# Performance work log

Measured on AMD Instinct MI355X. Metric: run time of the kernel, lower is better.

Reference implementation:

```python
import jax, jax.numpy as jnp
from jax import lax
import numpy as np

B, T, NX, NXS, NY, NYS, H = 4096, 60, 4, 3, 4, 3, 128


def lstm(x, h0, c0, Wih, Whh, bih, bhh):
    """PyTorch-convention LSTM. x: [B,T,D] -> (hs [B,T,H], hT, cT). Gate order i,f,g,o."""
    xg = jnp.einsum('btd,gd->btg', x, Wih) + bih  # [B,T,4H] precomputed input gates

    def step(carry, xg_t):
        h, c = carry
        g = xg_t + h @ Whh.T + bhh
        i, f, gg, o = jnp.split(g, 4, axis=-1)
        c = jax.nn.sigmoid(f) * c + jax.nn.sigmoid(i) * jnp.tanh(gg)
        h = jax.nn.sigmoid(o) * jnp.tanh(c)
        return (h, c), h

    (hT, cT), hs = lax.scan(step, (h0, c0), jnp.swapaxes(xg, 0, 1))
    return jnp.swapaxes(hs, 0, 1), hT, cT


def setup_inputs() -> dict:
    key = jax.random.key(0)
    ks = jax.random.split(key, 24)
    s = 0.1  # weight init scale
    inp = {
        'inputs_main': jax.random.normal(ks[0], (B, T, NX), jnp.float32),
        'inputs_sfc': jax.random.normal(ks[1], (B, NXS), jnp.float32),
        'rnn1_mem': jax.random.normal(ks[2], (B, T, H), jnp.float32),
        'hx2': jax.random.normal(ks[3], (B, H), jnp.float32),
        'cx2': jax.random.normal(ks[4], (B, H), jnp.float32),
        # surface MLPs -> initial h/c of rnn1
        'W_sfc1': s * jax.random.normal(ks[5], (H, NXS), jnp.float32),
        'b_sfc1': s * jax.random.normal(ks[6], (H,), jnp.float32),
        'W_sfc2': s * jax.random.normal(ks[7], (H, NXS), jnp.float32),
        'b_sfc2': s * jax.random.normal(ks[8], (H,), jnp.float32),
        # rnn1: input dim nx + nh_mem = 4 + 128 = 132
        'Wih1': s * jax.random.normal(ks[9], (4 * H, NX + H), jnp.float32),
        'Whh1': s * jax.random.normal(ks[10], (4 * H, H), jnp.float32),
        'bih1': s * jax.random.normal(ks[11], (4 * H,), jnp.float32),
        'bhh1': s * jax.random.normal(ks[12], (4 * H,), jnp.float32),
        # rnn2: input dim H
        'Wih2': s * jax.random.normal(ks[13], (4 * H, H), jnp.float32),
        'Whh2': s * jax.random.normal(ks[14], (4 * H, H), jnp.float32),
        'bih2': s * jax.random.normal(ks[15], (4 * H,), jnp.float32),
        'bhh2': s * jax.random.normal(ks[16], (4 * H,), jnp.float32),
        # intermediate + output MLPs
        'W_lat': s * jax.random.normal(ks[17], (H, H), jnp.float32),
        'b_lat': s * jax.random.normal(ks[18], (H,), jnp.float32),
        'W_out': s * jax.random.normal(ks[19], (NY, H), jnp.float32),
        'b_out': s * jax.random.normal(ks[20], (NY,), jnp.float32),
        'W_so': s * jax.random.normal(ks[21], (NYS, H), jnp.float32),
        'b_so': s * jax.random.normal(ks[22], (NYS,), jnp.float32),
    }
    return inp


def reference(inputs_main, inputs_sfc, rnn1_mem, hx2, cx2,
              W_sfc1, b_sfc1, W_sfc2, b_sfc2,
              Wih1, Whh1, bih1, bhh1,
              Wih2, Whh2, bih2, bhh2,
              W_lat, b_lat, W_out, b_out, W_so, b_so):
    # initial states of rnn1 from surface features
    hx = jnp.tanh(inputs_sfc @ W_sfc1.T + b_sfc1)
    cx = jnp.tanh(inputs_sfc @ W_sfc2.T + b_sfc2)
    # flip vertical levels, concat memory feedback
    x = jnp.flip(inputs_main, axis=1)
    x = jnp.concatenate([x, rnn1_mem], axis=2)  # [B,T,NX+H]
    rnn1out, _, _ = lstm(x, hx, cx, Wih1, Whh1, bih1, bhh1)
    rnn1out = jnp.flip(rnn1out, axis=1)
    # second LSTM over the opposite direction, random initial state
    rnn2out, last_h, _ = lstm(rnn1out, hx2, cx2, Wih2, Whh2, bih2, bhh2)
    # intermediate mlp (also becomes next-step memory in the stateful module)
    lat = rnn2out @ W_lat.T + b_lat  # [B,T,H]
    out = lat @ W_out.T + b_out      # [B,T,NY]
    out_sfc = last_h @ W_so.T + b_so  # [B,NYS]
    return out, out_sfc
```

## Files before the change

### kernel.cpp

```cpp
#include <hip/hip_runtime.h>
#include <stdint.h>


typedef __bf16 bf16x8 __attribute__((ext_vector_type(8)));
typedef __bf16 bf16x4 __attribute__((ext_vector_type(4)));
typedef float  f32x4  __attribute__((ext_vector_type(4)));

#define HQ      4096u
#define H0_OFF  0u
#define XD_OFF  8192u
#define XA_OFF  24576u
#define LDS_SZ  32256

#define S1f (-1.4426950408889634f)
#define S2f (-2.8853900817779268f)

__device__ __forceinline__ bf16x8 ldw8s(const float* __restrict__ p, float s){
  float4 a = *(const float4*)p;
  float4 b = *(const float4*)(p+4);
  bf16x8 r;
  r[0]=(__bf16)(a.x*s); r[1]=(__bf16)(a.y*s); r[2]=(__bf16)(a.z*s); r[3]=(__bf16)(a.w*s);
  r[4]=(__bf16)(b.x*s); r[5]=(__bf16)(b.y*s); r[6]=(__bf16)(b.z*s); r[7]=(__bf16)(b.w*s);
  return r;
}
__device__ __forceinline__ void load_wgate(bf16x8 (&dst)[8], const float* pih, const float* phh, int gg, float s){
  #pragma unroll
  for (int kk=0;kk<4;++kk) dst[kk]   = ldw8s(pih + kk*32 + gg*8, s);
  #pragma unroll
  for (int kk=0;kk<4;++kk) dst[4+kk] = ldw8s(phh + kk*32 + gg*8, s);
}
__device__ __forceinline__ void step_barrier(){
  asm volatile("s_waitcnt lgkmcnt(0)\n\ts_barrier" ::: "memory");
}
__device__ __forceinline__ void lstm_pw(const f32x4& a0, const f32x4& a1,
                                        const f32x4& a2, const f32x4& a3,
                                        float (&c_)[4], float (&hn)[4]){
  #pragma unroll
  for (int i=0;i<4;++i){
    float ei = __builtin_amdgcn_exp2f(a0[i]);
    float ef = __builtin_amdgcn_exp2f(a1[i]);
    float eg = __builtin_amdgcn_exp2f(fminf(a2[i], 126.0f));
    float eo = __builtin_amdgcn_exp2f(a3[i]);
    float sf = __builtin_amdgcn_rcpf(1.0f + ef);
    float itg = (1.0f - eg) * __builtin_amdgcn_rcpf((1.0f + ei)*(1.0f + eg));
    float ci = sf*c_[i] + itg;
    float ec = __builtin_amdgcn_exp2f(S2f*__builtin_fabsf(ci));
    float th = (1.0f - ec) * __builtin_amdgcn_rcpf((1.0f + eo)*(1.0f + ec));
    c_[i] = ci;
    hn[i] = __builtin_copysignf(th, ci);
  }
}

__global__ void comb_kernel(const float* __restrict__ W_lat, const float* __restrict__ b_lat,
                            const float* __restrict__ W_out, const float* __restrict__ b_out,
                            float* __restrict__ wcomb){
  int tid = threadIdx.x;
  int m = tid >> 7, k = tid & 127;
  float s = 0.f;
  for (int a=0;a<128;++a) s += W_out[m*128+a]*W_lat[a*128+k];
  wcomb[tid] = s;
  if (tid < 4){
    float sb = b_out[tid];
    for (int a=0;a<128;++a) sb += W_out[tid*128+a]*b_lat[a];
    wcomb[512+tid] = sb;
  }
}

#define MF(af_,wb_,ac_) ac_ = __builtin_amdgcn_mfma_f32_16x16x32_bf16(af_, wb_, ac_, 0,0,0)
#define BC8(q_) __builtin_bit_cast(bf16x8, q_)

#define BODY2(T_, CUR_, X0_,X1_,X2_,X3_) { \
    const uint32_t Hc_ = H0_OFF + (uint32_t)(CUR_)*HQ; \
    uint4 qh0_ = *(const uint4*)(lds + Hc_ + ((abase       ) ^ amask)); \
    uint4 qh1_ = *(const uint4*)(lds + Hc_ + ((abase +  64u) ^ amask)); \
    uint4 qh2_ = *(const uint4*)(lds + Hc_ + ((abase + 128u) ^ amask)); \
    uint4 qh3_ = *(const uint4*)(lds + Hc_ + ((abase + 192u) ^ amask)); \
    f32x4 a0 = biasv0, a1 = biasv1, a2 = biasv2, a3 = biasv3; \
    MF(BC8(X0_),wB0[0],a0); MF(BC8(X0_),wB1[0],a1); MF(BC8(X0_),wB2[0],a2); MF(BC8(X0_),wB3[0],a3); \
    MF(BC8(X1_),wB0[1],a0); MF(BC8(X1_),wB1[1],a1); MF(BC8(X1_),wB2[1],a2); MF(BC8(X1_),wB3[1],a3); \
    MF(BC8(X2_),wB0[2],a0); MF(BC8(X2_),wB1[2],a1); MF(BC8(X2_),wB2[2],a2); MF(BC8(X2_),wB3[2],a3); \
    MF(BC8(X3_),wB0[3],a0); MF(BC8(X3_),wB1[3],a1); MF(BC8(X3_),wB2[3],a2); MF(BC8(X3_),wB3[3],a3); \
    if ((T_) <= 57){ \
      const char* xp_ = wsb + (size_t)(57-(T_))*4096u + xfoff; \
      X0_ = *(const uint4*)(xp_);      X1_ = *(const uint4*)(xp_+64); \
      X2_ = *(const uint4*)(xp_+128);  X3_ = *(const uint4*)(xp_+192); \
    } \
    bf16x8 h0_ = BC8(qh0_), h1_ = BC8(qh1_), h2_ = BC8(qh2_), h3_ = BC8(qh3_); \
    MF(h0_,wB0[4],a0); MF(h0_,wB1[4],a1); MF(h0_,wB2[4],a2); MF(h0_,wB3[4],a3); \
    MF(h1_,wB0[5],a0); MF(h1_,wB1[5],a1); MF(h1_,wB2[5],a2); MF(h1_,wB3[5],a3); \
    MF(h2_,wB0[6],a0); MF(h2_,wB1[6],a1); MF(h2_,wB2[6],a2); MF(h2_,wB3[6],a3); \
    MF(h3_,wB0[7],a0); MF(h3_,wB1[7],a1); MF(h3_,wB2[7],a2); MF(h3_,wB3[7],a3); \
    f32x4 ao_ = {0.f,0.f,0.f,0.f}; \
    if (w == 0){ MF(h0_,wcB[0],ao_); MF(h1_,wcB[1],ao_); MF(h2_,wcB[2],ao_); MF(h3_,wcB[3],ao_); } \
    float hn_[4]; \
    lstm_pw(a0,a1,a2,a3, c_, hn_); \
    if ((T_) > 0 && w == 0 && l16 < 4){ \
      _Pragma("unroll") \
      for (int i_=0;i_<4;++i_) \
        dout[(size_t)(b0 + gg*4 + i_)*240 + (size_t)((T_)-1)*4 + l16] = ao_[i_] + bc; \
    } \
    _Pragma("unroll") \
    for (int i_=0;i_<4;++i_) \
      *(__bf16*)(lds + H0_OFF + (uint32_t)(1-(CUR_))*HQ + hw_off[i_]) = (__bf16)hn_[i_]; \
    step_barrier(); \
  }

__global__ __launch_bounds__(512, 2)
void lstm_fused(const float* __restrict__ xmain_g, const float* __restrict__ sfc,
                const float* __restrict__ mem_g, const float* __restrict__ hx2g,
                const float* __restrict__ cx2g,
                const float* __restrict__ Wsfc1, const float* __restrict__ bsfc1,
                const float* __restrict__ Wsfc2, const float* __restrict__ bsfc2,
                const float* __restrict__ Wih1, const float* __restrict__ Whh1,
                const float* __restrict__ bih1, const float* __restrict__ bhh1,
                const float* __restrict__ Wih2, const float* __restrict__ Whh2,
                const float* __restrict__ bih2, const float* __restrict__ bhh2,
                const float* __restrict__ Wso, const float* __restrict__ bso,
                const float* __restrict__ wcomb_ws,
                uint2* __restrict__ ws_u2, float* __restrict__ dout)
{
  __shared__ __align__(16) unsigned char lds[LDS_SZ];
  const int tid = threadIdx.x;
  const int w   = tid >> 6;
  const int l   = tid & 63;
  const int gg  = l >> 4;
  const int l16 = l & 15;
  const int blk = blockIdx.x;
  const int b0  = blk * 16;
  const int j   = (w<<4) + l16;
  const uint32_t amask = (uint32_t)((l16 & 7) << 4);
  const uint32_t abase = (uint32_t)(l16*256 + gg*16);
  const int srow = tid >> 5;
  const uint32_t stg_off = (uint32_t)(((srow*256) + (tid&31)*8) ^ ((srow&7)<<4));
  uint32_t hw_off[4];
  #pragma unroll
  for (int i=0;i<4;++i){
    int r = gg*4 + i;
    hw_off[i] = (uint32_t)((r*256 + j*2) ^ ((r&7)<<4));
  }
  uint2* wsimg = ws_u2 + (size_t)blk * 30720;
  const uint32_t imgoff = (uint32_t)(srow*32 + (tid&31));
  const char* wsb = (const char*)(ws_u2 + (size_t)blk * 30720);
  const uint32_t xfoff = (uint32_t)(l16*256 + gg*16);

  #pragma unroll
  for (int e = tid; e < 960; e += 512){
    int t = e >> 4, row = e & 15;
    float4 xv = *(const float4*)(xmain_g + (size_t)(b0+row)*240 + t*4);
    bf16x4 b4; b4[0]=(__bf16)xv.x; b4[1]=(__bf16)xv.y; b4[2]=(__bf16)xv.z; b4[3]=(__bf16)xv.w;
    *(bf16x4*)(lds + XA_OFF + (uint32_t)e*8u) = b4;
  }
  const float* memrow = mem_g + (size_t)(b0 + srow)*7680 + (tid&31)*4;
  {
    float4 m0 = *(const float4*)memrow;
    float4 m1 = *(const float4*)(memrow + 128);
    bf16x4 a4; a4[0]=(__bf16)m0.x; a4[1]=(__bf16)m0.y; a4[2]=(__bf16)m0.z; a4[3]=(__bf16)m0.w;
    bf16x4 b4; b4[0]=(__bf16)m1.x; b4[1]=(__bf16)m1.y; b4[2]=(__bf16)m1.z; b4[3]=(__bf16)m1.w;
    *(bf16x4*)(lds + XD_OFF + stg_off) = a4;
    *(bf16x4*)(lds + XD_OFF + HQ + stg_off) = b4;
  }
  {
    int c0 = (tid&31)*4;
    float4 wa = *(const float4*)(Wsfc1 + c0*3);
    float4 wb = *(const float4*)(Wsfc1 + c0*3 + 4);
    float4 wc = *(const float4*)(Wsfc1 + c0*3 + 8);
    const float* sp = sfc + (size_t)(b0+srow)*3;
    float s0 = sp[0], s1 = sp[1], s2 = sp[2];
    float4 bb = *(const float4*)(bsfc1 + c0);
    float v0 = tanhf(bb.x + s0*wa.x + s1*wa.y + s2*wa.z);
    float v1 = tanhf(bb.y + s0*wa.w + s1*wb.x + s2*wb.y);
    float v2 = tanhf(bb.z + s0*wb.z + s1*wb.w + s2*wc.x);
    float v3 = tanhf(bb.w + s0*wc.y + s1*wc.z + s2*wc.w);
    bf16x4 h4; h4[0]=(__bf16)v0; h4[1]=(__bf16)v1; h4[2]=(__bf16)v2; h4[3]=(__bf16)v3;
    *(bf16x4*)(lds + H0_OFF + stg_off) = h4;
  }
  float c_[4];
  {
    const float* wr = Wsfc2 + j*3;
    float w0_=wr[0], w1_=wr[1], w2_=wr[2];
    float bj = bsfc2[j];
    #pragma unroll
    for (int i=0;i<4;++i){
      const float* sp = sfc + (size_t)(b0 + gg*4 + i)*3;
      c_[i] = tanhf(bj + sp[0]*w0_ + sp[1]*w1_ + sp[2]*w2_);
    }
  }
  bf16x8 wB0[8], wB1[8], wB2[8], wB3[8];
  load_wgate(wB0, Wih1 + 4 + (size_t)(0*128+j)*132, Whh1 + (size_t)(0*128+j)*128, gg, S1f);
  load_wgate(wB1, Wih1 + 4 + (size_t)(1*128+j)*132, Whh1 + (size_t)(1*128+j)*128, gg, S1f);
  load_wgate(wB2, Wih1 + 4 + (size_t)(2*128+j)*132, Whh1 + (size_t)(2*128+j)*128, gg, S2f);
  load_wgate(wB3, Wih1 + 4 + (size_t)(3*128+j)*132, Whh1 + (size_t)(3*128+j)*128, gg, S1f);
  bf16x8 wxB0 = {}, wxB1 = {}, wxB2 = {}, wxB3 = {};
  if (gg == 0){
    float4 x0 = *(const float4*)(Wih1 + (size_t)(0*128+j)*132);
    float4 x1 = *(const float4*)(Wih1 + (size_t)(1*128+j)*132);
    float4 x2 = *(const float4*)(Wih1 + (size_t)(2*128+j)*132);
    float4 x3 = *(const float4*)(Wih1 + (size_t)(3*128+j)*132);
    wxB0[0]=(__bf16)(x0.x*S1f); wxB0[1]=(__bf16)(x0.y*S1f); wxB0[2]=(__bf16)(x0.z*S1f); wxB0[3]=(__bf16)(x0.w*S1f);
    wxB1[0]=(__bf16)(x1.x*S1f); wxB1[1]=(__bf16)(x1.y*S1f); wxB1[2]=(__bf16)(x1.z*S1f); wxB1[3]=(__bf16)(x1.w*S1f);
    wxB2[0]=(__bf16)(x2.x*S2f); wxB2[1]=(__bf16)(x2.y*S2f); wxB2[2]=(__bf16)(x2.z*S2f); wxB2[3]=(__bf16)(x2.w*S2f);
    wxB3[0]=(__bf16)(x3.x*S1f); wxB3[1]=(__bf16)(x3.y*S1f); wxB3[2]=(__bf16)(x3.z*S1f); wxB3[3]=(__bf16)(x3.w*S1f);
  }
  float bias0 = (bih1[0*128+j] + bhh1[0*128+j])*S1f;
  float bias1 = (bih1[1*128+j] + bhh1[1*128+j])*S1f;
  float bias2 = (bih1[2*128+j] + bhh1[2*128+j])*S2f;
  float bias3 = (bih1[3*128+j] + bhh1[3*128+j])*S1f;
  f32x4 biasv0 = {bias0,bias0,bias0,bias0};
  f32x4 biasv1 = {bias1,bias1,bias1,bias1};
  f32x4 biasv2 = {bias2,bias2,bias2,bias2};
  f32x4 biasv3 = {bias3,bias3,bias3,bias3};
  float4 P0 = *(const float4*)(memrow + 2*128);
  float4 P1 = *(const float4*)(memrow + 3*128);
  step_barrier();

  #pragma unroll 1
  for (int t=0; t<60; ++t){
    const uint32_t cur = (uint32_t)(t & 1);
    const uint32_t Hc = H0_OFF + cur*HQ;
    const uint32_t xb = XD_OFF + (uint32_t)(t & 3)*HQ;
    uint4 qx0 = *(const uint4*)(lds + xb + ((abase       ) ^ amask));
    uint4 qx1 = *(const uint4*)(lds + xb + ((abase +  64u) ^ amask));
    uint4 qx2 = *(const uint4*)(lds + xb + ((abase + 128u) ^ amask));
    uint4 qx3 = *(const uint4*)(lds + xb + ((abase + 192u) ^ amask));
    uint4 qh0 = *(const uint4*)(lds + Hc + ((abase       ) ^ amask));
    uint4 qh1 = *(const uint4*)(lds + Hc + ((abase +  64u) ^ amask));
    uint4 qh2 = *(const uint4*)(lds + Hc + ((abase + 128u) ^ amask));
    uint4 qh3 = *(const uint4*)(lds + Hc + ((abase + 192u) ^ amask));
    uint2 hv  = *(const uint2*)(lds + Hc + stg_off);
    bf16x8 xa = {};
    if (gg == 0){
      bf16x4 x4 = *(const bf16x4*)(lds + XA_OFF + (uint32_t)(((59-t)<<4) + l16)*8u);
      xa[0]=x4[0]; xa[1]=x4[1]; xa[2]=x4[2]; xa[3]=x4[3];
    }
    f32x4 a0 = biasv0, a1 = biasv1, a2 = biasv2, a3 = biasv3;
    MF(xa,wxB0,a0); MF(xa,wxB1,a1); MF(xa,wxB2,a2); MF(xa,wxB3,a3);
    MF(BC8(qx0),wB0[0],a0); MF(BC8(qx0),wB1[0],a1); MF(BC8(qx0),wB2[0],a2); MF(BC8(qx0),wB3[0],a3);
    MF(BC8(qx1),wB0[1],a0); MF(BC8(qx1),wB1[1],a1); MF(BC8(qx1),wB2[1],a2); MF(BC8(qx1),wB3[1],a3);
    MF(BC8(qx2),wB0[2],a0); MF(BC8(qx2),wB1[2],a1); MF(BC8(qx2),wB2[2],a2); MF(BC8(qx2),wB3[2],a3);
    MF(BC8(qx3),wB0[3],a0); MF(BC8(qx3),wB1[3],a1); MF(BC8(qx3),wB2[3],a2); MF(BC8(qx3),wB3[3],a3);
    bf16x8 h0 = BC8(qh0), h1 = BC8(qh1), h2 = BC8(qh2), h3 = BC8(qh3);
    MF(h0,wB0[4],a0); MF(h0,wB1[4],a1); MF(h0,wB2[4],a2); MF(h0,wB3[4],a3);
    MF(h1,wB0[5],a0); MF(h1,wB1[5],a1); MF(h1,wB2[5],a2); MF(h1,wB3[5],a3);
    MF(h2,wB0[6],a0); MF(h2,wB1[6],a1); MF(h2,wB2[6],a2); MF(h2,wB3[6],a3);
    MF(h3,wB0[7],a0); MF(h3,wB1[7],a1); MF(h3,wB2[7],a2); MF(h3,wB3[7],a3);
    float hn[4];
    lstm_pw(a0,a1,a2,a3, c_, hn);
    if (t >= 1) wsimg[(size_t)(t-1)*512 + imgoff] = hv;
    if (t + 2 <= 59){
      bf16x4 m4; m4[0]=(__bf16)P0.x; m4[1]=(__bf16)P0.y; m4[2]=(__bf16)P0.z; m4[3]=(__bf16)P0.w;
      *(bf16x4*)(lds + XD_OFF + (uint32_t)((t+2)&3)*HQ + stg_off) = m4;
    }
    #pragma unroll
    for (int i=0;i<4;++i)
      *(__bf16*)(lds + H0_OFF + (1u-cur)*HQ + hw_off[i]) = (__bf16)hn[i];
    P0 = P1;
    if (t + 4 <= 59) P1 = *(const float4*)(memrow + (size_t)(t+4)*128);
    step_barrier();
  }
  {
    uint2 hv = *(const uint2*)(lds + H0_OFF + stg_off);
    wsimg[(size_t)59*512 + imgoff] = hv;
    float4 h2v = *(const float4*)(hx2g + (size_t)(b0+srow)*128 + (tid&31)*4);
    bf16x4 h4; h4[0]=(__bf16)h2v.x; h4[1]=(__bf16)h2v.y; h4[2]=(__bf16)h2v.z; h4[3]=(__bf16)h2v.w;
    *(bf16x4*)(lds + H0_OFF + stg_off) = h4;
  }
  #pragma unroll
  for (int i=0;i<4;++i) c_[i] = cx2g[(size_t)(b0 + gg*4 + i)*128 + j];
  load_wgate(wB0, Wih2 + (size_t)(0*128+j)*128, Whh2 + (size_t)(0*128+j)*128, gg, S1f);
  load_wgate(wB1, Wih2 + (size_t)(1*128+j)*128, Whh2 + (size_t)(1*128+j)*128, gg, S1f);
  load_wgate(wB2, Wih2 + (size_t)(2*128+j)*128, Whh2 + (size_t)(2*128+j)*128, gg, S2f);
  load_wgate(wB3, Wih2 + (size_t)(3*128+j)*128, Whh2 + (size_t)(3*128+j)*128, gg, S1f);
  {
    float nb0 = (bih2[0*128+j] + bhh2[0*128+j])*S1f;
    float nb1 = (bih2[1*128+j] + bhh2[1*128+j])*S1f;
    float nb2 = (bih2[2*128+j] + bhh2[2*128+j])*S2f;
    float nb3 = (bih2[3*128+j] + bhh2[3*128+j])*S1f;
    biasv0 = (f32x4){nb0,nb0,nb0,nb0};
    biasv1 = (f32x4){nb1,nb1,nb1,nb1};
    biasv2 = (f32x4){nb2,nb2,nb2,nb2};
    biasv3 = (f32x4){nb3,nb3,nb3,nb3};
  }
  bf16x8 wcB[4] = {};
  if (w == 0){
    #pragma unroll
    for (int kk=0;kk<4;++kk){
      bf16x8 v = {};
      if (l16 < 4) v = ldw8s(wcomb_ws + l16*128 + kk*32 + gg*8, 1.0f);
      wcB[kk] = v;
    }
  }
  const float bc = (l16 < 4) ? wcomb_ws[512 + l16] : 0.f;
  asm volatile("s_waitcnt vmcnt(0) lgkmcnt(0)" ::: "memory");
  __builtin_amdgcn_s_barrier();

  uint4 xA0, xA1, xA2, xA3, xB0t, xB1t, xB2t, xB3t;
  {
    const char* pa = wsb + (size_t)59*4096u + xfoff;
    const char* pb = wsb + (size_t)58*4096u + xfoff;
    xA0 = *(const uint4*)(pa);     xA1 = *(const uint4*)(pa+64);
    xA2 = *(const uint4*)(pa+128); xA3 = *(const uint4*)(pa+192);
    xB0t = *(const uint4*)(pb);     xB1t = *(const uint4*)(pb+64);
    xB2t = *(const uint4*)(pb+128); xB3t = *(const uint4*)(pb+192);
  }

  #pragma unroll 1
  for (int tb = 0; tb < 60; tb += 2){
    BODY2(tb,   0, xA0,xA1,xA2,xA3)
    BODY2(tb+1, 1, xB0t,xB1t,xB2t,xB3t)
  }

  if (w == 0){
    bf16x8 wsB[4];
    #pragma unroll
    for (int kk=0;kk<4;++kk){
      bf16x8 v = {};
      if (l16 < 3) v = ldw8s(Wso + l16*128 + kk*32 + gg*8, 1.0f);
      wsB[kk] = v;
    }
    f32x4 ao = {0.f,0.f,0.f,0.f};
    f32x4 as_ = {0.f,0.f,0.f,0.f};
    #pragma unroll
    for (int kk=0;kk<4;++kk){
      uint4 q = *(const uint4*)(lds + H0_OFF + ((abase + 64u*(uint32_t)kk) ^ amask));
      bf16x8 af = BC8(q);
      MF(af, wcB[kk], ao);
      MF(af, wsB[kk], as_);
    }
    if (l16 < 4){
      #pragma unroll
      for (int i=0;i<4;++i)
        dout[(size_t)(b0 + gg*4 + i)*240 + 59*4 + l16] = ao[i] + bc;
    }
    if (l16 < 3){
      float bs = bso[l16];
      #pragma unroll
      for (int i=0;i<4;++i)
        dout[983040 + (size_t)(b0 + gg*4 + i)*3 + l16] = as_[i] + bs;
    }
  }
}

extern "C" void kernel_launch(void* const* d_in, const int* in_sizes, int n_in,
                              void* d_out, int out_size, void* d_ws, size_t ws_size,
                              hipStream_t stream){
  const float* inputs_main = (const float*)d_in[0];
  const float* inputs_sfc  = (const float*)d_in[1];
  const float* rnn1_mem    = (const float*)d_in[2];
  const float* hx2  = (const float*)d_in[3];
  const float* cx2  = (const float*)d_in[4];
  const float* W_sfc1 = (const float*)d_in[5];
  const float* b_sfc1 = (const float*)d_in[6];
  const float* W_sfc2 = (const float*)d_in[7];
  const float* b_sfc2 = (const float*)d_in[8];
  const float* Wih1 = (const float*)d_in[9];
  const float* Whh1 = (const float*)d_in[10];
  const float* bih1 = (const float*)d_in[11];
  const float* bhh1 = (const float*)d_in[12];
  const float* Wih2 = (const float*)d_in[13];
  const float* Whh2 = (const float*)d_in[14];
  const float* bih2 = (const float*)d_in[15];
  const float* bhh2 = (const float*)d_in[16];
  const float* W_lat = (const float*)d_in[17];
  const float* b_lat = (const float*)d_in[18];
  const float* W_out = (const float*)d_in[19];
  const float* b_out = (const float*)d_in[20];
  const float* W_so  = (const float*)d_in[21];
  const float* b_so  = (const float*)d_in[22];
  float* out = (float*)d_out;
  uint2* ws_u2 = (uint2*)d_ws;
  float* wcomb = (float*)((char*)d_ws + 62914560u);

  comb_kernel<<<dim3(1), dim3(512), 0, stream>>>(W_lat, b_lat, W_out, b_out, wcomb);
  lstm_fused<<<dim3(256), dim3(512), 0, stream>>>(inputs_main, inputs_sfc, rnn1_mem, hx2, cx2,
      W_sfc1, b_sfc1, W_sfc2, b_sfc2, Wih1, Whh1, bih1, bhh1, Wih2, Whh2, bih2, bhh2,
      W_so, b_so, wcomb, ws_u2, out);
}
```

Before: 228.0 us.

## Split block into recurrent and input-projection warp groups with LDS handoff

Doubles the block to 1024 threads. Warps 0-7 run only the recurrent h·Whh matmul and the pointwise update. Warps 8-15 precompute the next step's input-gate partials (x·Wih + bias) into a double-buffered LDS region, and also handle memory staging, the workspace writes and the output projection. The goal is to take the input-projection MFMAs off the serial critical path of each timestep. In exchange it uses much more LDS (about 104KB), allows only one block per CU instead of two, and adds an f32 partial round trip through LDS every step.

```diff
diff --git a/kernel.cpp b/kernel.cpp
--- a/kernel.cpp
+++ b/kernel.cpp
@@ -8,9 +8,12 @@
 
 #define HQ      4096u
 #define H0_OFF  0u
-#define XD_OFF  8192u
-#define XA_OFF  24576u
-#define LDS_SZ  32256
+#define PART    8192u
+#define PHALF   32768u
+#define XD_OFF  73728u
+#define XA_OFF  90112u
+#define WC_OFF  97792u
+#define LDS_SZ  105984
 
 #define S1f (-1.4426950408889634f)
 #define S2f (-2.8853900817779268f)
@@ -23,11 +26,9 @@
   r[4]=(__bf16)(b.x*s); r[5]=(__bf16)(b.y*s); r[6]=(__bf16)(b.z*s); r[7]=(__bf16)(b.w*s);
   return r;
 }
-__device__ __forceinline__ void load_wgate(bf16x8 (&dst)[8], const float* pih, const float* phh, int gg, float s){
+__device__ __forceinline__ void load_w4(bf16x8 (&dst)[4], const float* __restrict__ p, int gg, float s){
   #pragma unroll
-  for (int kk=0;kk<4;++kk) dst[kk]   = ldw8s(pih + kk*32 + gg*8, s);
-  #pragma unroll
-  for (int kk=0;kk<4;++kk) dst[4+kk] = ldw8s(phh + kk*32 + gg*8, s);
+  for (int kk=0;kk<4;++kk) dst[kk] = ldw8s(p + kk*32 + gg*8, s);
 }
 __device__ __forceinline__ void step_barrier(){
   asm volatile("s_waitcnt lgkmcnt(0)\n\ts_barrier" ::: "memory");
@@ -69,43 +70,7 @@
 #define MF(af_,wb_,ac_) ac_ = __builtin_amdgcn_mfma_f32_16x16x32_bf16(af_, wb_, ac_, 0,0,0)
 #define BC8(q_) __builtin_bit_cast(bf16x8, q_)
 
-#define BODY2(T_, CUR_, X0_,X1_,X2_,X3_) { \
-    const uint32_t Hc_ = H0_OFF + (uint32_t)(CUR_)*HQ; \
-    uint4 qh0_ = *(const uint4*)(lds + Hc_ + ((abase       ) ^ amask)); \
-    uint4 qh1_ = *(const uint4*)(lds + Hc_ + ((abase +  64u) ^ amask)); \
-    uint4 qh2_ = *(const uint4*)(lds + Hc_ + ((abase + 128u) ^ amask)); \
-    uint4 qh3_ = *(const uint4*)(lds + Hc_ + ((abase + 192u) ^ amask)); \
-    f32x4 a0 = biasv0, a1 = biasv1, a2 = biasv2, a3 = biasv3; \
-    MF(BC8(X0_),wB0[0],a0); MF(BC8(X0_),wB1[0],a1); MF(BC8(X0_),wB2[0],a2); MF(BC8(X0_),wB3[0],a3); \
-    MF(BC8(X1_),wB0[1],a0); MF(BC8(X1_),wB1[1],a1); MF(BC8(X1_),wB2[1],a2); MF(BC8(X1_),wB3[1],a3); \
-    MF(BC8(X2_),wB0[2],a0); MF(BC8(X2_),wB1[2],a1); MF(BC8(X2_),wB2[2],a2); MF(BC8(X2_),wB3[2],a3); \
-    MF(BC8(X3_),wB0[3],a0); MF(BC8(X3_),wB1[3],a1); MF(BC8(X3_),wB2[3],a2); MF(BC8(X3_),wB3[3],a3); \
-    if ((T_) <= 57){ \
-      const char* xp_ = wsb + (size_t)(57-(T_))*4096u + xfoff; \
-      X0_ = *(const uint4*)(xp_);      X1_ = *(const uint4*)(xp_+64); \
-      X2_ = *(const uint4*)(xp_+128);  X3_ = *(const uint4*)(xp_+192); \
-    } \
-    bf16x8 h0_ = BC8(qh0_), h1_ = BC8(qh1_), h2_ = BC8(qh2_), h3_ = BC8(qh3_); \
-    MF(h0_,wB0[4],a0); MF(h0_,wB1[4],a1); MF(h0_,wB2[4],a2); MF(h0_,wB3[4],a3); \
-    MF(h1_,wB0[5],a0); MF(h1_,wB1[5],a1); MF(h1_,wB2[5],a2); MF(h1_,wB3[5],a3); \
-    MF(h2_,wB0[6],a0); MF(h2_,wB1[6],a1); MF(h2_,wB2[6],a2); MF(h2_,wB3[6],a3); \
-    MF(h3_,wB0[7],a0); MF(h3_,wB1[7],a1); MF(h3_,wB2[7],a2); MF(h3_,wB3[7],a3); \
-    f32x4 ao_ = {0.f,0.f,0.f,0.f}; \
-    if (w == 0){ MF(h0_,wcB[0],ao_); MF(h1_,wcB[1],ao_); MF(h2_,wcB[2],ao_); MF(h3_,wcB[3],ao_); } \
-    float hn_[4]; \
-    lstm_pw(a0,a1,a2,a3, c_, hn_); \
-    if ((T_) > 0 && w == 0 && l16 < 4){ \
-      _Pragma("unroll") \
-      for (int i_=0;i_<4;++i_) \
-        dout[(size_t)(b0 + gg*4 + i_)*240 + (size_t)((T_)-1)*4 + l16] = ao_[i_] + bc; \
-    } \
-    _Pragma("unroll") \
-    for (int i_=0;i_<4;++i_) \
-      *(__bf16*)(lds + H0_OFF + (uint32_t)(1-(CUR_))*HQ + hw_off[i_]) = (__bf16)hn_[i_]; \
-    step_barrier(); \
-  }
-
-__global__ __launch_bounds__(512, 2)
+__global__ __launch_bounds__(1024, 1)
 void lstm_fused(const float* __restrict__ xmain_g, const float* __restrict__ sfc,
                 const float* __restrict__ mem_g, const float* __restrict__ hx2g,
                 const float* __restrict__ cx2g,
@@ -127,215 +92,322 @@
   const int l16 = l & 15;
   const int blk = blockIdx.x;
   const int b0  = blk * 16;
-  const int j   = (w<<4) + l16;
   const uint32_t amask = (uint32_t)((l16 & 7) << 4);
   const uint32_t abase = (uint32_t)(l16*256 + gg*16);
-  const int srow = tid >> 5;
-  const uint32_t stg_off = (uint32_t)(((srow*256) + (tid&31)*8) ^ ((srow&7)<<4));
-  uint32_t hw_off[4];
+  uint2* wsimg = ws_u2 + (size_t)blk * 30720;
+  const char* wsb = (const char*)wsimg;
+
   #pragma unroll
-  for (int i=0;i<4;++i){
-    int r = gg*4 + i;
-    hw_off[i] = (uint32_t)((r*256 + j*2) ^ ((r&7)<<4));
-  }
-  uint2* wsimg = ws_u2 + (size_t)blk * 30720;
-  const uint32_t imgoff = (uint32_t)(srow*32 + (tid&31));
-  const char* wsb = (const char*)(ws_u2 + (size_t)blk * 30720);
-  const uint32_t xfoff = (uint32_t)(l16*256 + gg*16);
-
-  #pragma unroll
-  for (int e = tid; e < 960; e += 512){
+  for (int e = tid; e < 960; e += 1024){
     int t = e >> 4, row = e & 15;
     float4 xv = *(const float4*)(xmain_g + (size_t)(b0+row)*240 + t*4);
     bf16x4 b4; b4[0]=(__bf16)xv.x; b4[1]=(__bf16)xv.y; b4[2]=(__bf16)xv.z; b4[3]=(__bf16)xv.w;
     *(bf16x4*)(lds + XA_OFF + (uint32_t)e*8u) = b4;
   }
-  const float* memrow = mem_g + (size_t)(b0 + srow)*7680 + (tid&31)*4;
-  {
-    float4 m0 = *(const float4*)memrow;
-    float4 m1 = *(const float4*)(memrow + 128);
-    bf16x4 a4; a4[0]=(__bf16)m0.x; a4[1]=(__bf16)m0.y; a4[2]=(__bf16)m0.z; a4[3]=(__bf16)m0.w;
-    bf16x4 b4; b4[0]=(__bf16)m1.x; b4[1]=(__bf16)m1.y; b4[2]=(__bf16)m1.z; b4[3]=(__bf16)m1.w;
-    *(bf16x4*)(lds + XD_OFF + stg_off) = a4;
-    *(bf16x4*)(lds + XD_OFF + HQ + stg_off) = b4;
-  }
-  {
-    int c0 = (tid&31)*4;
-    float4 wa = *(const float4*)(Wsfc1 + c0*3);
-    float4 wb = *(const float4*)(Wsfc1 + c0*3 + 4);
-    float4 wc = *(const float4*)(Wsfc1 + c0*3 + 8);
-    const float* sp = sfc + (size_t)(b0+srow)*3;
-    float s0 = sp[0], s1 = sp[1], s2 = sp[2];
-    float4 bb = *(const float4*)(bsfc1 + c0);
-    float v0 = tanhf(bb.x + s0*wa.x + s1*wa.y + s2*wa.z);
-    float v1 = tanhf(bb.y + s0*wa.w + s1*wb.x + s2*wb.y);
-    float v2 = tanhf(bb.z + s0*wb.z + s1*wb.w + s2*wc.x);
-    float v3 = tanhf(bb.w + s0*wc.y + s1*wc.z + s2*wc.w);
-    bf16x4 h4; h4[0]=(__bf16)v0; h4[1]=(__bf16)v1; h4[2]=(__bf16)v2; h4[3]=(__bf16)v3;
-    *(bf16x4*)(lds + H0_OFF + stg_off) = h4;
-  }
-  float c_[4];
-  {
-    const float* wr = Wsfc2 + j*3;
-    float w0_=wr[0], w1_=wr[1], w2_=wr[2];
-    float bj = bsfc2[j];
+
+  if (tid < 512){
+    const int j = w*16 + l16;
+    const int srow = tid >> 5;
+    const uint32_t stg_off = (uint32_t)(((srow*256) + (tid&31)*8) ^ ((srow&7)<<4));
+    uint32_t hw_off[4];
     #pragma unroll
     for (int i=0;i<4;++i){
-      const float* sp = sfc + (size_t)(b0 + gg*4 + i)*3;
-      c_[i] = tanhf(bj + sp[0]*w0_ + sp[1]*w1_ + sp[2]*w2_);
-    }
-  }
-  bf16x8 wB0[8], wB1[8], wB2[8], wB3[8];
-  load_wgate(wB0, Wih1 + 4 + (size_t)(0*128+j)*132, Whh1 + (size_t)(0*128+j)*128, gg, S1f);
-  load_wgate(wB1, Wih1 + 4 + (size_t)(1*128+j)*132, Whh1 + (size_t)(1*128+j)*128, gg, S1f);
-  load_wgate(wB2, Wih1 + 4 + (size_t)(2*128+j)*132, Whh1 + (size_t)(2*128+j)*128, gg, S2f);
-  load_wgate(wB3, Wih1 + 4 + (size_t)(3*128+j)*132, Whh1 + (size_t)(3*128+j)*128, gg, S1f);
-  bf16x8 wxB0 = {}, wxB1 = {}, wxB2 = {}, wxB3 = {};
-  if (gg == 0){
-    float4 x0 = *(const float4*)(Wih1 + (size_t)(0*128+j)*132);
-    float4 x1 = *(const float4*)(Wih1 + (size_t)(1*128+j)*132);
-    float4 x2 = *(const float4*)(Wih1 + (size_t)(2*128+j)*132);
-    float4 x3 = *(const float4*)(Wih1 + (size_t)(3*128+j)*132);
-    wxB0[0]=(__bf16)(x0.x*S1f); wxB0[1]=(__bf16)(x0.y*S1f); wxB0[2]=(__bf16)(x0.z*S1f); wxB0[3]=(__bf16)(x0.w*S1f);
-    wxB1[0]=(__bf16)(x1.x*S1f); wxB1[1]=(__bf16)(x1.y*S1f); wxB1[2]=(__bf16)(x1.z*S1f); wxB1[3]=(__bf16)(x1.w*S1f);
-    wxB2[0]=(__bf16)(x2.x*S2f); wxB2[1]=(__bf16)(x2.y*S2f); wxB2[2]=(__bf16)(x2.z*S2f); wxB2[3]=(__bf16)(x2.w*S2f);
-    wxB3[0]=(__bf16)(x3.x*S1f); wxB3[1]=(__bf16)(x3.y*S1f); wxB3[2]=(__bf16)(x3.z*S1f); wxB3[3]=(__bf16)(x3.w*S1f);
-  }
-  float bias0 = (bih1[0*128+j] + bhh1[0*128+j])*S1f;
-  float bias1 = (bih1[1*128+j] + bhh1[1*128+j])*S1f;
-  float bias2 = (bih1[2*128+j] + bhh1[2*128+j])*S2f;
-  float bias3 = (bih1[3*128+j] + bhh1[3*128+j])*S1f;
-  f32x4 biasv0 = {bias0,bias0,bias0,bias0};
-  f32x4 biasv1 = {bias1,bias1,bias1,bias1};
-  f32x4 biasv2 = {bias2,bias2,bias2,bias2};
-  f32x4 biasv3 = {bias3,bias3,bias3,bias3};
-  float4 P0 = *(const float4*)(memrow + 2*128);
-  float4 P1 = *(const float4*)(memrow + 3*128);
-  step_barrier();
-
-  #pragma unroll 1
-  for (int t=0; t<60; ++t){
-    const uint32_t cur = (uint32_t)(t & 1);
-    const uint32_t Hc = H0_OFF + cur*HQ;
-    const uint32_t xb = XD_OFF + (uint32_t)(t & 3)*HQ;
-    uint4 qx0 = *(const uint4*)(lds + xb + ((abase       ) ^ amask));
-    uint4 qx1 = *(const uint4*)(lds + xb + ((abase +  64u) ^ amask));
-    uint4 qx2 = *(const uint4*)(lds + xb + ((abase + 128u) ^ amask));
-    uint4 qx3 = *(const uint4*)(lds + xb + ((abase + 192u) ^ amask));
-    uint4 qh0 = *(const uint4*)(lds + Hc + ((abase       ) ^ amask));
-    uint4 qh1 = *(const uint4*)(lds + Hc + ((abase +  64u) ^ amask));
-    uint4 qh2 = *(const uint4*)(lds + Hc + ((abase + 128u) ^ amask));
-    uint4 qh3 = *(const uint4*)(lds + Hc + ((abase + 192u) ^ amask));
-    uint2 hv  = *(const uint2*)(lds + Hc + stg_off);
-    bf16x8 xa = {};
+      int r = gg*4 + i;
+      hw_off[i] = (uint32_t)((r*256 + j*2) ^ ((r&7)<<4));
+    }
+    {
+      int c0 = (tid&31)*4;
+      float4 wa = *(const float4*)(Wsfc1 + c0*3);
+      float4 wb = *(const float4*)(Wsfc1 + c0*3 + 4);
+      float4 wc = *(const float4*)(Wsfc1 + c0*3 + 8);
+      const float* sp = sfc + (size_t)(b0+srow)*3;
+      float s0 = sp[0], s1 = sp[1], s2 = sp[2];
+      float4 bb = *(const float4*)(bsfc1 + c0);
+      float v0 = tanhf(bb.x + s0*wa.x + s1*wa.y + s2*wa.z);
+      float v1 = tanhf(bb.y + s0*wa.w + s1*wb.x + s2*wb.y);
+      float v2 = tanhf(bb.z + s0*wb.z + s1*wb.w + s2*wc.x);
+      float v3 = tanhf(bb.w + s0*wc.y + s1*wc.z + s2*wc.w);
+      bf16x4 h4; h4[0]=(__bf16)v0; h4[1]=(__bf16)v1; h4[2]=(__bf16)v2; h4[3]=(__bf16)v3;
+      *(bf16x4*)(lds + H0_OFF + stg_off) = h4;
+    }
+    float c_[4];
+    {
+      const float* wr = Wsfc2 + j*3;
+      float w0_=wr[0], w1_=wr[1], w2_=wr[2];
+      float bj = bsfc2[j];
+      #pragma unroll
+      for (int i=0;i<4;++i){
+        const float* sp = sfc + (size_t)(b0 + gg*4 + i)*3;
+        c_[i] = tanhf(bj + sp[0]*w0_ + sp[1]*w1_ + sp[2]*w2_);
+      }
+    }
+    bf16x8 wB0[4], wB1[4], wB2[4], wB3[4];
+    load_w4(wB0, Whh1 + (size_t)(0*128+j)*128, gg, S1f);
+    load_w4(wB1, Whh1 + (size_t)(1*128+j)*128, gg, S1f);
+    load_w4(wB2, Whh1 + (size_t)(2*128+j)*128, gg, S2f);
+    load_w4(wB3, Whh1 + (size_t)(3*128+j)*128, gg, S1f);
+    step_barrier();
+    step_barrier();
+    #pragma unroll 1
+    for (int t=0; t<60; ++t){
+      const uint32_t Hc = H0_OFF + (uint32_t)(t&1)*HQ;
+      const uint32_t Pc = PART + (uint32_t)(t&1)*PHALF + (uint32_t)tid*64u;
+      f32x4 a0 = *(const f32x4*)(lds + Pc);
+      f32x4 a1 = *(const f32x4*)(lds + Pc + 16);
+      f32x4 a2 = *(const f32x4*)(lds + Pc + 32);
+      f32x4 a3 = *(const f32x4*)(lds + Pc + 48);
+      uint4 qh0 = *(const uint4*)(lds + Hc + ((abase       ) ^ amask));
+      uint4 qh1 = *(const uint4*)(lds + Hc + ((abase +  64u) ^ amask));
+      uint4 qh2 = *(const uint4*)(lds + Hc + ((abase + 128u) ^ amask));
+      uint4 qh3 = *(const uint4*)(lds + Hc + ((abase + 192u) ^ amask));
+      bf16x8 h0 = BC8(qh0), h1 = BC8(qh1), h2 = BC8(qh2), h3 = BC8(qh3);
+      MF(h0,wB0[0],a0); MF(h0,wB1[0],a1); MF(h0,wB2[0],a2); MF(h0,wB3[0],a3);
+      MF(h1,wB0[1],a0); MF(h1,wB1[1],a1); MF(h1,wB2[1],a2); MF(h1,wB3[1],a3);
+      MF(h2,wB0[2],a0); MF(h2,wB1[2],a1); MF(h2,wB2[2],a2); MF(h2,wB3[2],a3);
+      MF(h3,wB0[3],a0); MF(h3,wB1[3],a1); MF(h3,wB2[3],a2); MF(h3,wB3[3],a3);
+      float hn[4];
+      lstm_pw(a0,a1,a2,a3, c_, hn);
+      #pragma unroll
+      for (int i=0;i<4;++i)
+        *(__bf16*)(lds + H0_OFF + (uint32_t)((t+1)&1)*HQ + hw_off[i]) = (__bf16)hn[i];
+      step_barrier();
+    }
+    load_w4(wB0, Whh2 + (size_t)(0*128+j)*128, gg, S1f);
+    load_w4(wB1, Whh2 + (size_t)(1*128+j)*128, gg, S1f);
+    load_w4(wB2, Whh2 + (size_t)(2*128+j)*128, gg, S2f);
+    load_w4(wB3, Whh2 + (size_t)(3*128+j)*128, gg, S1f);
+    #pragma unroll
+    for (int i=0;i<4;++i) c_[i] = cx2g[(size_t)(b0 + gg*4 + i)*128 + j];
+    step_barrier();
+    {
+      float4 h2v = *(const float4*)(hx2g + (size_t)(b0+srow)*128 + (tid&31)*4);
+      bf16x4 h4; h4[0]=(__bf16)h2v.x; h4[1]=(__bf16)h2v.y; h4[2]=(__bf16)h2v.z; h4[3]=(__bf16)h2v.w;
+      *(bf16x4*)(lds + H0_OFF + stg_off) = h4;
+    }
+    step_barrier();
+    #pragma unroll 1
+    for (int t=0; t<60; ++t){
+      const uint32_t Hc = H0_OFF + (uint32_t)(t&1)*HQ;
+      const uint32_t Pc = PART + (uint32_t)(t&1)*PHALF + (uint32_t)tid*64u;
+      f32x4 a0 = *(const f32x4*)(lds + Pc);
+      f32x4 a1 = *(const f32x4*)(lds + Pc + 16);
+      f32x4 a2 = *(const f32x4*)(lds + Pc + 32);
+      f32x4 a3 = *(const f32x4*)(lds + Pc + 48);
+      uint4 qh0 = *(const uint4*)(lds + Hc + ((abase       ) ^ amask));
+      uint4 qh1 = *(const uint4*)(lds + Hc + ((abase +  64u) ^ amask));
+      uint4 qh2 = *(const uint4*)(lds + Hc + ((abase + 128u) ^ amask));
+      uint4 qh3 = *(const uint4*)(lds + Hc + ((abase + 192u) ^ amask));
+      bf16x8 h0 = BC8(qh0), h1 = BC8(qh1), h2 = BC8(qh2), h3 = BC8(qh3);
+      MF(h0,wB0[0],a0); MF(h0,wB1[0],a1); MF(h0,wB2[0],a2); MF(h0,wB3[0],a3);
+      MF(h1,wB0[1],a0); MF(h1,wB1[1],a1); MF(h1,wB2[1],a2); MF(h1,wB3[1],a3);
+      MF(h2,wB0[2],a0); MF(h2,wB1[2],a1); MF(h2,wB2[2],a2); MF(h2,wB3[2],a3);
+      MF(h3,wB0[3],a0); MF(h3,wB1[3],a1); MF(h3,wB2[3],a2); MF(h3,wB3[3],a3);
+      float hn[4];
+      lstm_pw(a0,a1,a2,a3, c_, hn);
+      #pragma unroll
+      for (int i=0;i<4;++i)
+        *(__bf16*)(lds + H0_OFF + (uint32_t)((t+1)&1)*HQ + hw_off[i]) = (__bf16)hn[i];
+      step_barrier();
+    }
+  } else {
+    const int xtid = tid - 512;
+    const int xw = w - 8;
+    const int j = xw*16 + l16;
+    const int srow = xtid >> 5;
+    const uint32_t stg_off = (uint32_t)(((srow*256) + (xtid&31)*8) ^ ((srow&7)<<4));
+    const uint32_t imgoff = (uint32_t)(srow*32 + (xtid&31));
+    const uint32_t xfoff = (uint32_t)(l16*256 + gg*16);
+    const float* memrow = mem_g + (size_t)(b0 + srow)*7680 + (xtid&31)*4;
+    {
+      float4 m0 = *(const float4*)memrow;
+      float4 m1 = *(const float4*)(memrow + 128);
+      bf16x4 a4; a4[0]=(__bf16)m0.x; a4[1]=(__bf16)m0.y; a4[2]=(__bf16)m0.z; a4[3]=(__bf16)m0.w;
+      bf16x4 b4; b4[0]=(__bf16)m1.x; b4[1]=(__bf16)m1.y; b4[2]=(__bf16)m1.z; b4[3]=(__bf16)m1.w;
+      *(bf16x4*)(lds + XD_OFF + stg_off) = a4;
+      *(bf16x4*)(lds + XD_OFF + HQ + stg_off) = b4;
+    }
+    bf16x8 wB0[4], wB1[4], wB2[4], wB3[4];
+    load_w4(wB0, Wih1 + 4 + (size_t)(0*128+j)*132, gg, S1f);
+    load_w4(wB1, Wih1 + 4 + (size_t)(1*128+j)*132, gg, S1f);
+    load_w4(wB2, Wih1 + 4 + (size_t)(2*128+j)*132, gg, S2f);
+    load_w4(wB3, Wih1 + 4 + (size_t)(3*128+j)*132, gg, S1f);
+    bf16x8 wxB0 = {}, wxB1 = {}, wxB2 = {}, wxB3 = {};
     if (gg == 0){
-      bf16x4 x4 = *(const bf16x4*)(lds + XA_OFF + (uint32_t)(((59-t)<<4) + l16)*8u);
-      xa[0]=x4[0]; xa[1]=x4[1]; xa[2]=x4[2]; xa[3]=x4[3];
-    }
-    f32x4 a0 = biasv0, a1 = biasv1, a2 = biasv2, a3 = biasv3;
-    MF(xa,wxB0,a0); MF(xa,wxB1,a1); MF(xa,wxB2,a2); MF(xa,wxB3,a3);
-    MF(BC8(qx0),wB0[0],a0); MF(BC8(qx0),wB1[0],a1); MF(BC8(qx0),wB2[0],a2); MF(BC8(qx0),wB3[0],a3);
-    MF(BC8(qx1),wB0[1],a0); MF(BC8(qx1),wB1[1],a1); MF(BC8(qx1),wB2[1],a2); MF(BC8(qx1),wB3[1],a3);
-    MF(BC8(qx2),wB0[2],a0); MF(BC8(qx2),wB1[2],a1); MF(BC8(qx2),wB2[2],a2); MF(BC8(qx2),wB3[2],a3);
-    MF(BC8(qx3),wB0[3],a0); MF(BC8(qx3),wB1[3],a1); MF(BC8(qx3),wB2[3],a2); MF(BC8(qx3),wB3[3],a3);
-    bf16x8 h0 = BC8(qh0), h1 = BC8(qh1), h2 = BC8(qh2), h3 = BC8(qh3);
-    MF(h0,wB0[4],a0); MF(h0,wB1[4],a1); MF(h0,wB2[4],a2); MF(h0,wB3[4],a3);
-    MF(h1,wB0[5],a0); MF(h1,wB1[5],a1); MF(h1,wB2[5],a2); MF(h1,wB3[5],a3);
-    MF(h2,wB0[6],a0); MF(h2,wB1[6],a1); MF(h2,wB2[6],a2); MF(h2,wB3[6],a3);
-    MF(h3,wB0[7],a0); MF(h3,wB1[7],a1); MF(h3,wB2[7],a2); MF(h3,wB3[7],a3);
-    float hn[4];
-    lstm_pw(a0,a1,a2,a3, c_, hn);
-    if (t >= 1) wsimg[(size_t)(t-1)*512 + imgoff] = hv;
-    if (t + 2 <= 59){
-      bf16x4 m4; m4[0]=(__bf16)P0.x; m4[1]=(__bf16)P0.y; m4[2]=(__bf16)P0.z; m4[3]=(__bf16)P0.w;
-      *(bf16x4*)(lds + XD_OFF + (uint32_t)((t+2)&3)*HQ + stg_off) = m4;
-    }
-    #pragma unroll
-    for (int i=0;i<4;++i)
-      *(__bf16*)(lds + H0_OFF + (1u-cur)*HQ + hw_off[i]) = (__bf16)hn[i];
-    P0 = P1;
-    if (t + 4 <= 59) P1 = *(const float4*)(memrow + (size_t)(t+4)*128);
-    step_barrier();
-  }
-  {
-    uint2 hv = *(const uint2*)(lds + H0_OFF + stg_off);
-    wsimg[(size_t)59*512 + imgoff] = hv;
-    float4 h2v = *(const float4*)(hx2g + (size_t)(b0+srow)*128 + (tid&31)*4);
-    bf16x4 h4; h4[0]=(__bf16)h2v.x; h4[1]=(__bf16)h2v.y; h4[2]=(__bf16)h2v.z; h4[3]=(__bf16)h2v.w;
-    *(bf16x4*)(lds + H0_OFF + stg_off) = h4;
-  }
-  #pragma unroll
-  for (int i=0;i<4;++i) c_[i] = cx2g[(size_t)(b0 + gg*4 + i)*128 + j];
-  load_wgate(wB0, Wih2 + (size_t)(0*128+j)*128, Whh2 + (size_t)(0*128+j)*128, gg, S1f);
-  load_wgate(wB1, Wih2 + (size_t)(1*128+j)*128, Whh2 + (size_t)(1*128+j)*128, gg, S1f);
-  load_wgate(wB2, Wih2 + (size_t)(2*128+j)*128, Whh2 + (size_t)(2*128+j)*128, gg, S2f);
-  load_wgate(wB3, Wih2 + (size_t)(3*128+j)*128, Whh2 + (size_t)(3*128+j)*128, gg, S1f);
-  {
-    float nb0 = (bih2[0*128+j] + bhh2[0*128+j])*S1f;
-    float nb1 = (bih2[1*128+j] + bhh2[1*128+j])*S1f;
-    float nb2 = (bih2[2*128+j] + bhh2[2*128+j])*S2f;
-    float nb3 = (bih2[3*128+j] + bhh2[3*128+j])*S1f;
-    biasv0 = (f32x4){nb0,nb0,nb0,nb0};
-    biasv1 = (f32x4){nb1,nb1,nb1,nb1};
-    biasv2 = (f32x4){nb2,nb2,nb2,nb2};
-    biasv3 = (f32x4){nb3,nb3,nb3,nb3};
-  }
-  bf16x8 wcB[4] = {};
-  if (w == 0){
-    #pragma unroll
-    for (int kk=0;kk<4;++kk){
-      bf16x8 v = {};
-      if (l16 < 4) v = ldw8s(wcomb_ws + l16*128 + kk*32 + gg*8, 1.0f);
-      wcB[kk] = v;
-    }
-  }
-  const float bc = (l16 < 4) ? wcomb_ws[512 + l16] : 0.f;
-  asm volatile("s_waitcnt vmcnt(0) lgkmcnt(0)" ::: "memory");
-  __builtin_amdgcn_s_barrier();
-
-  uint4 xA0, xA1, xA2, xA3, xB0t, xB1t, xB2t, xB3t;
-  {
-    const char* pa = wsb + (size_t)59*4096u + xfoff;
-    const char* pb = wsb + (size_t)58*4096u + xfoff;
-    xA0 = *(const uint4*)(pa);     xA1 = *(const uint4*)(pa+64);
-    xA2 = *(const uint4*)(pa+128); xA3 = *(const uint4*)(pa+192);
-    xB0t = *(const uint4*)(pb);     xB1t = *(const uint4*)(pb+64);
-    xB2t = *(const uint4*)(pb+128); xB3t = *(const uint4*)(pb+192);
-  }
-
-  #pragma unroll 1
-  for (int tb = 0; tb < 60; tb += 2){
-    BODY2(tb,   0, xA0,xA1,xA2,xA3)
-    BODY2(tb+1, 1, xB0t,xB1t,xB2t,xB3t)
-  }
-
-  if (w == 0){
-    bf16x8 wsB[4];
-    #pragma unroll
-    for (int kk=0;kk<4;++kk){
-      bf16x8 v = {};
-      if (l16 < 3) v = ldw8s(Wso + l16*128 + kk*32 + gg*8, 1.0f);
-      wsB[kk] = v;
-    }
-    f32x4 ao = {0.f,0.f,0.f,0.f};
-    f32x4 as_ = {0.f,0.f,0.f,0.f};
-    #pragma unroll
-    for (int kk=0;kk<4;++kk){
-      uint4 q = *(const uint4*)(lds + H0_OFF + ((abase + 64u*(uint32_t)kk) ^ amask));
-      bf16x8 af = BC8(q);
-      MF(af, wcB[kk], ao);
-      MF(af, wsB[kk], as_);
-    }
-    if (l16 < 4){
-      #pragma unroll
-      for (int i=0;i<4;++i)
-        dout[(size_t)(b0 + gg*4 + i)*240 + 59*4 + l16] = ao[i] + bc;
-    }
-    if (l16 < 3){
-      float bs = bso[l16];
-      #pragma unroll
-      for (int i=0;i<4;++i)
-        dout[983040 + (size_t)(b0 + gg*4 + i)*3 + l16] = as_[i] + bs;
+      float4 x0 = *(const float4*)(Wih1 + (size_t)(0*128+j)*132);
+      float4 x1 = *(const float4*)(Wih1 + (size_t)(1*128+j)*132);
+      float4 x2 = *(const float4*)(Wih1 + (size_t)(2*128+j)*132);
+      float4 x3 = *(const float4*)(Wih1 + (size_t)(3*128+j)*132);
+      wxB0[0]=(__bf16)(x0.x*S1f); wxB0[1]=(__bf16)(x0.y*S1f); wxB0[2]=(__bf16)(x0.z*S1f); wxB0[3]=(__bf16)(x0.w*S1f);
+      wxB1[0]=(__bf16)(x1.x*S1f); wxB1[1]=(__bf16)(x1.y*S1f); wxB1[2]=(__bf16)(x1.z*S1f); wxB1[3]=(__bf16)(x1.w*S1f);
+      wxB2[0]=(__bf16)(x2.x*S2f); wxB2[1]=(__bf16)(x2.y*S2f); wxB2[2]=(__bf16)(x2.z*S2f); wxB2[3]=(__bf16)(x2.w*S2f);
+      wxB3[0]=(__bf16)(x3.x*S1f); wxB3[1]=(__bf16)(x3.y*S1f); wxB3[2]=(__bf16)(x3.z*S1f); wxB3[3]=(__bf16)(x3.w*S1f);
+    }
+    float b0s = (bih1[0*128+j] + bhh1[0*128+j])*S1f;
+    float b1s = (bih1[1*128+j] + bhh1[1*128+j])*S1f;
+    float b2s = (bih1[2*128+j] + bhh1[2*128+j])*S2f;
+    float b3s = (bih1[3*128+j] + bhh1[3*128+j])*S1f;
+    float4 P0 = *(const float4*)(memrow + 2*128);
+    float4 P1 = *(const float4*)(memrow + 3*128);
+    step_barrier();
+    {
+      f32x4 a0={b0s,b0s,b0s,b0s}, a1={b1s,b1s,b1s,b1s}, a2={b2s,b2s,b2s,b2s}, a3={b3s,b3s,b3s,b3s};
+      bf16x8 xa = {};
+      if (gg == 0){
+        bf16x4 x4 = *(const bf16x4*)(lds + XA_OFF + (uint32_t)((59<<4) + l16)*8u);
+        xa[0]=x4[0]; xa[1]=x4[1]; xa[2]=x4[2]; xa[3]=x4[3];
+      }
+      MF(xa,wxB0,a0); MF(xa,wxB1,a1); MF(xa,wxB2,a2); MF(xa,wxB3,a3);
+      #pragma unroll
+      for (int kk=0;kk<4;++kk){
+        uint4 q = *(const uint4*)(lds + XD_OFF + ((abase + 64u*(uint32_t)kk) ^ amask));
+        bf16x8 af = BC8(q);
+        MF(af,wB0[kk],a0); MF(af,wB1[kk],a1); MF(af,wB2[kk],a2); MF(af,wB3[kk],a3);
+      }
+      const uint32_t pc = PART + (uint32_t)xtid*64u;
+      *(f32x4*)(lds + pc)      = a0;
+      *(f32x4*)(lds + pc + 16) = a1;
+      *(f32x4*)(lds + pc + 32) = a2;
+      *(f32x4*)(lds + pc + 48) = a3;
+    }
+    step_barrier();
+    #pragma unroll 1
+    for (int t=0; t<60; ++t){
+      if (t >= 1){
+        uint2 hv = *(const uint2*)(lds + H0_OFF + (uint32_t)(t&1)*HQ + stg_off);
+        wsimg[(size_t)(t-1)*512 + imgoff] = hv;
+      }
+      if (t < 59){
+        f32x4 a0={b0s,b0s,b0s,b0s}, a1={b1s,b1s,b1s,b1s}, a2={b2s,b2s,b2s,b2s}, a3={b3s,b3s,b3s,b3s};
+        bf16x8 xa = {};
+        if (gg == 0){
+          bf16x4 x4 = *(const bf16x4*)(lds + XA_OFF + (uint32_t)(((58-t)<<4) + l16)*8u);
+          xa[0]=x4[0]; xa[1]=x4[1]; xa[2]=x4[2]; xa[3]=x4[3];
+        }
+        MF(xa,wxB0,a0); MF(xa,wxB1,a1); MF(xa,wxB2,a2); MF(xa,wxB3,a3);
+        const uint32_t xb = XD_OFF + (uint32_t)((t+1)&3)*HQ;
+        #pragma unroll
+        for (int kk=0;kk<4;++kk){
+          uint4 q = *(const uint4*)(lds + xb + ((abase + 64u*(uint32_t)kk) ^ amask));
+          bf16x8 af = BC8(q);
+          MF(af,wB0[kk],a0); MF(af,wB1[kk],a1); MF(af,wB2[kk],a2); MF(af,wB3[kk],a3);
+        }
+        const uint32_t pc = PART + (uint32_t)((t+1)&1)*PHALF + (uint32_t)xtid*64u;
+        *(f32x4*)(lds + pc)      = a0;
+        *(f32x4*)(lds + pc + 16) = a1;
+        *(f32x4*)(lds + pc + 32) = a2;
+        *(f32x4*)(lds + pc + 48) = a3;
+      }
+      if (t + 2 <= 59){
+        bf16x4 m4; m4[0]=(__bf16)P0.x; m4[1]=(__bf16)P0.y; m4[2]=(__bf16)P0.z; m4[3]=(__bf16)P0.w;
+        *(bf16x4*)(lds + XD_OFF + (uint32_t)((t+2)&3)*HQ + stg_off) = m4;
+      }
+      P0 = P1;
+      if (t + 4 <= 59) P1 = *(const float4*)(memrow + (size_t)(t+4)*128);
+      step_barrier();
+    }
+    {
+      uint2 hv = *(const uint2*)(lds + H0_OFF + stg_off);
+      wsimg[(size_t)59*512 + imgoff] = hv;
+      load_w4(wB0, Wih2 + (size_t)(0*128+j)*128, gg, S1f);
+      load_w4(wB1, Wih2 + (size_t)(1*128+j)*128, gg, S1f);
+      load_w4(wB2, Wih2 + (size_t)(2*128+j)*128, gg, S2f);
+      load_w4(wB3, Wih2 + (size_t)(3*128+j)*128, gg, S1f);
+      b0s = (bih2[0*128+j] + bhh2[0*128+j])*S1f;
+      b1s = (bih2[1*128+j] + bhh2[1*128+j])*S1f;
+      b2s = (bih2[2*128+j] + bhh2[2*128+j])*S2f;
+      b3s = (bih2[3*128+j] + bhh2[3*128+j])*S1f;
+      f32x4 a0={b0s,b0s,b0s,b0s}, a1={b1s,b1s,b1s,b1s}, a2={b2s,b2s,b2s,b2s}, a3={b3s,b3s,b3s,b3s};
+      #pragma unroll
+      for (int kk=0;kk<4;++kk){
+        uint4 q = *(const uint4*)(lds + H0_OFF + ((abase + 64u*(uint32_t)kk) ^ amask));
+        bf16x8 af = BC8(q);
+        MF(af,wB0[kk],a0); MF(af,wB1[kk],a1); MF(af,wB2[kk],a2); MF(af,wB3[kk],a3);
+      }
+      const uint32_t pc = PART + (uint32_t)xtid*64u;
+      *(f32x4*)(lds + pc)      = a0;
+      *(f32x4*)(lds + pc + 16) = a1;
+      *(f32x4*)(lds + pc + 32) = a2;
+      *(f32x4*)(lds + pc + 48) = a3;
+      if (xtid < 512){
+        float v = wcomb_ws[xtid];
+        *(__bf16*)(lds + WC_OFF + (uint32_t)xtid*2u) = (__bf16)v;
+      }
+      asm volatile("s_waitcnt vmcnt(0)" ::: "memory");
+    }
+    step_barrier();
+    uint4 X0, X1, X2, X3;
+    {
+      const char* xp = wsb + (size_t)58*4096u + xfoff;
+      X0 = *(const uint4*)(xp);      X1 = *(const uint4*)(xp+64);
+      X2 = *(const uint4*)(xp+128);  X3 = *(const uint4*)(xp+192);
+    }
+    const float bc = (l16 < 4) ? wcomb_ws[512 + l16] : 0.f;
+    step_barrier();
+    #pragma unroll 1
+    for (int t=0; t<60; ++t){
+      if (t >= 1 && w == 8){
+        const uint32_t Hc = H0_OFF + (uint32_t)(t&1)*HQ;
+        f32x4 ao = {0.f,0.f,0.f,0.f};
+        #pragma unroll
+        for (int kk=0;kk<4;++kk){
+          uint4 qh = *(const uint4*)(lds + Hc + ((abase + 64u*(uint32_t)kk) ^ amask));
+          uint4 qw = *(const uint4*)(lds + WC_OFF + (uint32_t)(l16*256 + gg*16 + kk*64));
+          ao = __builtin_amdgcn_mfma_f32_16x16x32_bf16(BC8(qh), BC8(qw), ao, 0,0,0);
+        }
+        if (l16 < 4){
+          #pragma unroll
+          for (int i=0;i<4;++i)
+            dout[(size_t)(b0 + gg*4 + i)*240 + (size_t)(t-1)*4 + l16] = ao[i] + bc;
+        }
+      }
+      if (t < 59){
+        f32x4 a0={b0s,b0s,b0s,b0s}, a1={b1s,b1s,b1s,b1s}, a2={b2s,b2s,b2s,b2s}, a3={b3s,b3s,b3s,b3s};
+        MF(BC8(X0),wB0[0],a0); MF(BC8(X0),wB1[0],a1); MF(BC8(X0),wB2[0],a2); MF(BC8(X0),wB3[0],a3);
+        MF(BC8(X1),wB0[1],a0); MF(BC8(X1),wB1[1],a1); MF(BC8(X1),wB2[1],a2); MF(BC8(X1),wB3[1],a3);
+        MF(BC8(X2),wB0[2],a0); MF(BC8(X2),wB1[2],a1); MF(BC8(X2),wB2[2],a2); MF(BC8(X2),wB3[2],a3);
+        MF(BC8(X3),wB0[3],a0); MF(BC8(X3),wB1[3],a1); MF(BC8(X3),wB2[3],a2); MF(BC8(X3),wB3[3],a3);
+        const uint32_t pc = PART + (uint32_t)((t+1)&1)*PHALF + (uint32_t)xtid*64u;
+        *(f32x4*)(lds + pc)      = a0;
+        *(f32x4*)(lds + pc + 16) = a1;
+        *(f32x4*)(lds + pc + 32) = a2;
+        *(f32x4*)(lds + pc + 48) = a3;
+        if (t <= 57){
+          const char* xp = wsb + (size_t)(57-t)*4096u + xfoff;
+          X0 = *(const uint4*)(xp);      X1 = *(const uint4*)(xp+64);
+          X2 = *(const uint4*)(xp+128);  X3 = *(const uint4*)(xp+192);
+        }
+      }
+      step_barrier();
+    }
+    if (w == 8){
+      bf16x8 wsB[4];
+      #pragma unroll
+      for (int kk=0;kk<4;++kk){
+        bf16x8 v = {};
+        if (l16 < 3) v = ldw8s(Wso + l16*128 + kk*32 + gg*8, 1.0f);
+        wsB[kk] = v;
+      }
+      f32x4 ao = {0.f,0.f,0.f,0.f};
+      f32x4 as_ = {0.f,0.f,0.f,0.f};
+      #pragma unroll
+      for (int kk=0;kk<4;++kk){
+        uint4 qh = *(const uint4*)(lds + H0_OFF + ((abase + 64u*(uint32_t)kk) ^ amask));
+        uint4 qw = *(const uint4*)(lds + WC_OFF + (uint32_t)(l16*256 + gg*16 + kk*64));
+        bf16x8 af = BC8(qh);
+        ao  = __builtin_amdgcn_mfma_f32_16x16x32_bf16(af, BC8(qw), ao, 0,0,0);
+        as_ = __builtin_amdgcn_mfma_f32_16x16x32_bf16(af, wsB[kk], as_, 0,0,0);
+      }
+      if (l16 < 4){
+        #pragma unroll
+        for (int i=0;i<4;++i)
+          dout[(size_t)(b0 + gg*4 + i)*240 + 59*4 + l16] = ao[i] + bc;
+      }
+      if (l16 < 3){
+        float bs = bso[l16];
+        #pragma unroll
+        for (int i=0;i<4;++i)
+          dout[983040 + (size_t)(b0 + gg*4 + i)*3 + l16] = as_[i] + bs;
+      }
     }
   }
 }
@@ -371,7 +443,7 @@
   float* wcomb = (float*)((char*)d_ws + 62914560u);
 
   comb_kernel<<<dim3(1), dim3(512), 0, stream>>>(W_lat, b_lat, W_out, b_out, wcomb);
-  lstm_fused<<<dim3(256), dim3(512), 0, stream>>>(inputs_main, inputs_sfc, rnn1_mem, hx2, cx2,
+  lstm_fused<<<dim3(256), dim3(1024), 0, stream>>>(inputs_main, inputs_sfc, rnn1_mem, hx2, cx2,
       W_sfc1, b_sfc1, W_sfc2, b_sfc2, Wih1, Whh1, bih1, bhh1, Wih2, Whh2, bih2, bhh2,
       W_so, b_so, wcomb, ws_u2, out);
 }
```

Result: slower. 294.9 us (+29.4%).
